# Kernel optimization log

Hardware: AMD Instinct MI355X
Metric: run time of the kernel (lower is better)

Reference implementation:

```python
import jax, jax.numpy as jnp
import numpy as np

N = 100000
FEAT = 32
RS, RT = 128, 100
BOUND = 1.6
K_A = -2.0 * np.log(0.2)  # thresholds from module-level constants
K_B = -2.0 * np.log(0.8)


def setup_inputs() -> dict:
    key = jax.random.key(0)
    ks = jax.random.split(key, 10)
    pts = jax.random.normal(ks[0], (N, 3), dtype=jnp.float32) * 0.5
    time = jax.random.uniform(ks[1], (N, 1), dtype=jnp.float32)
    # build well-conditioned SPD covariances, then extract the 6 unique entries
    A = jax.random.normal(ks[2], (N, 3, 3), dtype=jnp.float32) * 0.3
    C = A @ jnp.swapaxes(A, 1, 2) + 0.05 * jnp.eye(3, dtype=jnp.float32)
    cov6 = jnp.stack([C[:, 0, 0], C[:, 0, 1], C[:, 0, 2],
                      C[:, 1, 1], C[:, 1, 2], C[:, 2, 2]], axis=-1)
    planes = {}
    shapes = {0: (FEAT, RS, RS), 1: (FEAT, RS, RS), 2: (FEAT, RS, RT),
              3: (FEAT, RS, RS), 4: (FEAT, RS, RT), 5: (FEAT, RS, RT)}
    for i in range(6):
        planes[f'plane{i}'] = jax.random.normal(ks[3 + i], shapes[i], dtype=jnp.float32) * 0.1
    return dict(pts=pts, time=time, cov6=cov6, **planes)


def _cov3x3(c6):
    # [N,6] -> symmetric [N,3,3]
    r0 = jnp.stack([c6[:, 0], c6[:, 1], c6[:, 2]], axis=-1)
    r1 = jnp.stack([c6[:, 1], c6[:, 3], c6[:, 4]], axis=-1)
    r2 = jnp.stack([c6[:, 2], c6[:, 4], c6[:, 5]], axis=-1)
    return jnp.stack([r0, r1, r2], axis=1)


def _structured_samples(pts, cov6):
    # faithful to structured_gaussian_samples (offsets computed under no_grad)
    sg = jax.lax.stop_gradient
    C = _cov3x3(sg(cov6))
    _, V = jnp.linalg.eigh(C)                      # eigenvectors as columns
    normals = V.reshape(-1, 3)                     # rows of V, as in .view(-1,1,3)
    Cinv = jnp.linalg.inv(C)
    Cinv_rep = jnp.repeat(Cinv, 3, axis=0)         # [3N,3,3]
    lam = jnp.einsum('ni,nij,nj->n', normals, Cinv_rep, normals)[:, None]
    p_a = jnp.sqrt(K_A / lam) * normals
    p_b = jnp.sqrt(K_B / lam) * normals
    o = jnp.repeat(sg(pts), 3, axis=0)             # [3N,3]
    x_a = sg((o + p_a).reshape(-1, 3, 3))
    x_b = sg((o + p_b).reshape(-1, 3, 3))
    x_an = sg((o - p_a).reshape(-1, 3, 3))
    x_bn = sg((o - p_b).reshape(-1, 3, 3))
    return jnp.concatenate([pts[:, None, :], x_a, x_b, x_an, x_bn], axis=1)  # [N,13,3]


def _bilinear(plane, coords):
    # plane [F,H,W]; coords [M,2] in [-1,1], coord0 -> W (x), coord1 -> H (y); align_corners=True
    F_, H, W = plane.shape
    x = (coords[:, 0] + 1.0) * 0.5 * (W - 1)
    y = (coords[:, 1] + 1.0) * 0.5 * (H - 1)
    x0 = jnp.floor(x); y0 = jnp.floor(y)
    wx = (x - x0)[:, None]; wy = (y - y0)[:, None]
    x0i = jnp.clip(x0, 0, W - 1).astype(jnp.int32)
    x1i = jnp.clip(x0 + 1, 0, W - 1).astype(jnp.int32)
    y0i = jnp.clip(y0, 0, H - 1).astype(jnp.int32)
    y1i = jnp.clip(y0 + 1, 0, H - 1).astype(jnp.int32)
    v00 = plane[:, y0i, x0i].T  # [M,F]
    v01 = plane[:, y0i, x1i].T
    v10 = plane[:, y1i, x0i].T
    v11 = plane[:, y1i, x1i].T
    return ((1 - wy) * ((1 - wx) * v00 + wx * v01)
            + wy * ((1 - wx) * v10 + wx * v11))


def _forward(pts, time, cov6, planes):
    M = 13
    samples = _structured_samples(pts, cov6)          # [N,13,3]
    t = time * 2.0 - 1.0
    t = jnp.tile(t, (samples.shape[1], 1))            # faithful to time.repeat(13,1)
    aabb_max = jnp.full((3,), BOUND, dtype=pts.dtype)
    aabb_min = jnp.full((3,), -BOUND, dtype=pts.dtype)
    s = (samples - aabb_max) * (2.0 / (aabb_min - aabb_max)) - 1.0  # normalize_aabb
    data = jnp.concatenate([s.reshape(-1, 3), t], axis=-1)  # [13N,4]
    coord_pairs = [(0, 1), (0, 2), (3, 0), (1, 2), (3, 1), (3, 2)]
    space = 1.0
    spacetime = 1.0
    for i, (q, r) in enumerate(coord_pairs):
        feat = _bilinear(planes[i], data[:, (q, r)])  # [13N,F]
        feat = feat.reshape(-1, M, feat.shape[-1]).mean(axis=1)  # [N,F]
        if i in (0, 1, 3):
            space = space * feat
        else:
            spacetime = spacetime * feat
    return space, spacetime


def reference(pts, time, cov6, plane0, plane1, plane2, plane3, plane4, plane5):
    space, spacetime = _forward(pts, time, cov6,
                                [plane0, plane1, plane2, plane3, plane4, plane5])
    coltime = jnp.ones((), dtype=space.dtype)
    return space, spacetime, coltime
```

## Files before the change

### kernel.cpp

```cpp
#include <hip/hip_runtime.h>
#include <hip/hip_fp16.h>
#include <stdint.h>

#define NP 100000
#define PPB 64
#define KA 3.2188758248682006f
#define KB 0.44628710262841953f
#define PSCALE 16.0f

#define SS_DW 131072
#define ST_DW 102400
#define OFF0 0
#define OFF1 (OFF0 + SS_DW)
#define OFF2 (OFF1 + SS_DW)
#define OFF3 (OFF2 + ST_DW)
#define OFF4 (OFF3 + SS_DW)
#define OFF5 (OFF4 + ST_DW)

typedef float v2f __attribute__((ext_vector_type(2)));
typedef __fp16 v2h __attribute__((ext_vector_type(2)));

__device__ __forceinline__ int clampi(int v, int hi){ v = v < 0 ? 0 : v; return v > hi ? hi : v; }

struct Dim { int i0, i1; float fr; };

__device__ __forceinline__ Dim mkdim(float g, int hi){
  float fl = floorf(g);
  Dim d;
  d.fr = g - fl;
  int i = (int)fl;
  d.i0 = clampi(i, hi);
  d.i1 = clampi(i + 1, hi);
  return d;
}

template<bool HI>
__device__ __forceinline__ __half2 dec8(uint32_t w){
#if __has_builtin(__builtin_amdgcn_cvt_scalef32_pk_f16_fp8)
  v2h h = __builtin_amdgcn_cvt_scalef32_pk_f16_fp8(w, 1.0f, HI);
  return __builtin_bit_cast(__half2, h);
#else
  v2f f = __builtin_amdgcn_cvt_pk_f32_fp8((int)w, HI);
  v2h h = __builtin_amdgcn_cvt_pkrtz(f.x, f.y);
  return __builtin_bit_cast(__half2, h);
#endif
}

__device__ __forceinline__ void row8(uint4 v, __half2 w, __half2* acc){
  acc[0] = __hfma2(dec8<false>(v.x), w, acc[0]);
  acc[1] = __hfma2(dec8<true >(v.x), w, acc[1]);
  acc[2] = __hfma2(dec8<false>(v.y), w, acc[2]);
  acc[3] = __hfma2(dec8<true >(v.y), w, acc[3]);
  acc[4] = __hfma2(dec8<false>(v.z), w, acc[4]);
  acc[5] = __hfma2(dec8<true >(v.z), w, acc[5]);
  acc[6] = __hfma2(dec8<false>(v.w), w, acc[6]);
  acc[7] = __hfma2(dec8<true >(v.w), w, acc[7]);
}

__device__ __forceinline__ void bilinpair(const uint4* __restrict__ P,
    int rA, int rB, int x0, __half2 wx, __half2 wyg, __half2 wyf,
    int fp, __half2* acc){
  uint4 vA = P[((rA + x0) << 1) + fp];
  uint4 vB = P[((rB + x0) << 1) + fp];
  __half2 wA = __hmul2(wyg, wx), wB = __hmul2(wyf, wx);
  row8(vA, wA, acc);
  row8(vB, wB, acc);
}

__device__ __forceinline__ float3 eigvec3(float c00,float c01,float c02,
                                          float c11,float c12,float c22,float lam){
  float m00 = c00 - lam, m11 = c11 - lam, m22 = c22 - lam;
  float ux0 = c01*c12 - c02*m11, uy0 = c02*c01 - m00*c12, uz0 = m00*m11 - c01*c01;
  float ux1 = c01*m22 - c02*c12, uy1 = c02*c02 - m00*m22, uz1 = m00*c12 - c01*c02;
  float ux2 = m11*m22 - c12*c12, uy2 = c12*c02 - c01*m22, uz2 = c01*c12 - m11*c02;
  float n0 = ux0*ux0 + uy0*uy0 + uz0*uz0;
  float n1 = ux1*ux1 + uy1*uy1 + uz1*uz1;
  float n2 = ux2*ux2 + uy2*uy2 + uz2*uz2;
  float ux = ux0, uy = uy0, uz = uz0, nn = n0;
  if (n1 > nn){ ux = ux1; uy = uy1; uz = uz1; nn = n1; }
  if (n2 > nn){ ux = ux2; uy = uy2; uz = uz2; nn = n2; }
  float inv = 1.0f / sqrtf(nn + 1e-45f);
  return make_float3(ux*inv, uy*inv, uz*inv);
}

__global__ __launch_bounds__(256) void wpf_transpose(
    const float* __restrict__ p0, const float* __restrict__ p1,
    const float* __restrict__ p2, const float* __restrict__ p3,
    const float* __restrict__ p4, const float* __restrict__ p5,
    uint32_t* __restrict__ ws, float* __restrict__ coltime)
{
  __shared__ float tile[32][65];
  int plane = blockIdx.y;
  if (plane == 0 && blockIdx.x == 0 && threadIdx.x == 0) coltime[0] = 1.0f;
  const float* src; int off, HW;
  switch (plane){
    case 0:  src = p0; off = OFF0; HW = 16384; break;
    case 1:  src = p1; off = OFF1; HW = 16384; break;
    case 2:  src = p2; off = OFF2; HW = 12800; break;
    case 3:  src = p3; off = OFF3; HW = 16384; break;
    case 4:  src = p4; off = OFF4; HW = 12800; break;
    default: src = p5; off = OFF5; HW = 12800; break;
  }
  int hw0 = blockIdx.x * 64;
  if (hw0 >= HW) return;
  int hwt = threadIdx.x & 63;
  int fq  = threadIdx.x >> 6;
  #pragma unroll
  for (int i = 0; i < 8; ++i){
    int f = fq * 8 + i;
    tile[f][hwt] = src[f * HW + hw0 + hwt];
  }
  __syncthreads();
  int d  = threadIdx.x & 7;
  int h2 = threadIdx.x >> 3;
  #pragma unroll
  for (int i = 0; i < 2; ++i){
    int hl = i * 32 + h2;
    float a = tile[4*d+0][hl] * PSCALE;
    float b = tile[4*d+1][hl] * PSCALE;
    float c = tile[4*d+2][hl] * PSCALE;
    float e = tile[4*d+3][hl] * PSCALE;
    int r = __builtin_amdgcn_cvt_pk_fp8_f32(a, b, 0, false);
    r     = __builtin_amdgcn_cvt_pk_fp8_f32(c, e, r, true);
    ws[off + (hw0 + hl) * 8 + d] = (uint32_t)r;
  }
}

__global__ __launch_bounds__(256, 4) void wpf_main(
    const float* __restrict__ pts, const float* __restrict__ tim,
    const float* __restrict__ cov6, const uint32_t* __restrict__ ws,
    float* __restrict__ out)
{
  __shared__ float4 smp[PPB][13];
  int tidl = threadIdx.x;
  int pbase = blockIdx.x * PPB;

  if (tidl < PPB){
    int pt = pbase + tidl;
    if (pt < NP){
      float px = pts[pt*3+0], py = pts[pt*3+1], pz = pts[pt*3+2];
      float c00 = cov6[pt*6+0], c01 = cov6[pt*6+1], c02 = cov6[pt*6+2];
      float c11 = cov6[pt*6+3], c12 = cov6[pt*6+4], c22 = cov6[pt*6+5];

      float q3 = (c00 + c11 + c22) * (1.0f/3.0f);
      float p1 = c01*c01 + c02*c02 + c12*c12;
      float d00 = c00 - q3, d11 = c11 - q3, d22 = c22 - q3;
      float p2 = d00*d00 + d11*d11 + d22*d22 + 2.0f*p1;
      float pp = sqrtf(p2 * (1.0f/6.0f)) + 1e-30f;
      float pinv = 1.0f / pp;
      float b00 = d00*pinv, b11 = d11*pinv, b22 = d22*pinv;
      float b01 = c01*pinv, b02 = c02*pinv, b12 = c12*pinv;
      float detB = b00*(b11*b22 - b12*b12) - b01*(b01*b22 - b12*b02) + b02*(b01*b12 - b11*b02);
      float r = fminf(1.0f, fmaxf(-1.0f, 0.5f * detB));
      float phi = acosf(r) * (1.0f/3.0f);
      float l2 = q3 + 2.0f*pp*cosf(phi);
      float l0 = q3 + 2.0f*pp*cosf(phi + 2.0943951023931953f);
      float3 v0 = eigvec3(c00,c01,c02,c11,c12,c22, l0);
      float3 v2 = eigvec3(c00,c01,c02,c11,c12,c22, l2);
      float v1x = v2.y*v0.z - v2.z*v0.y;
      float v1y = v2.z*v0.x - v2.x*v0.z;
      float v1z = v2.x*v0.y - v2.y*v0.x;
      float v1inv = 1.0f / sqrtf(v1x*v1x + v1y*v1y + v1z*v1z + 1e-45f);
      v1x *= v1inv; v1y *= v1inv; v1z *= v1inv;

      float nx[3] = { v0.x, v0.y, v0.z };
      float ny[3] = { v1x,  v1y,  v1z  };
      float nz[3] = { v2.x, v2.y, v2.z };

      float A00 = c11*c22 - c12*c12;
      float A01 = c02*c12 - c01*c22;
      float A02 = c01*c12 - c02*c11;
      float A11 = c00*c22 - c02*c02;
      float A12 = c01*c02 - c00*c12;
      float A22 = c00*c11 - c01*c01;
      float det  = c00*A00 + c01*A01 + c02*A02;
      float dinv = 1.0f / det;
      float i00 = A00*dinv, i01 = A01*dinv, i02 = A02*dinv;
      float i11 = A11*dinv, i12 = A12*dinv, i22 = A22*dinv;

      float gpx = fmaf(px, -39.6875f, 63.5f);
      float gpy = fmaf(py, -39.6875f, 63.5f);
      float gpz = fmaf(pz, -39.6875f, 63.5f);
      float axA[3], ayA[3], azA[3], axB[3], ayB[3], azB[3];
      #pragma unroll
      for (int k = 0; k < 3; ++k){
        float a = nx[k], b = ny[k], c = nz[k];
        float lam = i00*a*a + i11*b*b + i22*c*c + 2.0f*(i01*a*b + i02*a*c + i12*b*c);
        float linv = 1.0f / lam;
        float sA = -39.6875f * sqrtf(KA * linv);
        float sB = -39.6875f * sqrtf(KB * linv);
        axA[k] = sA*a; ayA[k] = sA*b; azA[k] = sA*c;
        axB[k] = sB*a; ayB[k] = sB*b; azB[k] = sB*c;
      }

      int tb = (pt * 13) % NP;
      int ti = tb;
      smp[tidl][0] = make_float4(gpx, gpy, gpz, tim[ti] * 99.0f);
      #pragma unroll
      for (int k = 0; k < 3; ++k){
        ti = tb + 1 + k; if (ti >= NP) ti -= NP;
        smp[tidl][1+k]  = make_float4(gpx+axA[k], gpy+ayA[k], gpz+azA[k], tim[ti]*99.0f);
      }
      #pragma unroll
      for (int k = 0; k < 3; ++k){
        ti = tb + 4 + k; if (ti >= NP) ti -= NP;
        smp[tidl][4+k]  = make_float4(gpx+axB[k], gpy+ayB[k], gpz+azB[k], tim[ti]*99.0f);
      }
      #pragma unroll
      for (int k = 0; k < 3; ++k){
        ti = tb + 7 + k; if (ti >= NP) ti -= NP;
        smp[tidl][7+k]  = make_float4(gpx-axA[k], gpy-ayA[k], gpz-azA[k], tim[ti]*99.0f);
      }
      #pragma unroll
      for (int k = 0; k < 3; ++k){
        ti = tb + 10 + k; if (ti >= NP) ti -= NP;
        smp[tidl][10+k] = make_float4(gpx-axB[k], gpy-ayB[k], gpz-azB[k], tim[ti]*99.0f);
      }
    }
  }
  __syncthreads();

  int lp = tidl >> 2, fp = tidl & 3;
  int pt = pbase + lp;
  if (pt >= NP) return;
  bool xhi = (fp & 2) != 0;

  const uint4* __restrict__ w0p = reinterpret_cast<const uint4*>(ws + OFF0);
  const uint4* __restrict__ w1p = reinterpret_cast<const uint4*>(ws + OFF1);
  const uint4* __restrict__ w2p = reinterpret_cast<const uint4*>(ws + OFF2);
  const uint4* __restrict__ w3p = reinterpret_cast<const uint4*>(ws + OFF3);
  const uint4* __restrict__ w4p = reinterpret_cast<const uint4*>(ws + OFF4);
  const uint4* __restrict__ w5p = reinterpret_cast<const uint4*>(ws + OFF5);

  __half2 acc[6][8];
  __half2 z = __float2half2_rn(0.0f);
  #pragma unroll
  for (int i = 0; i < 6; ++i)
    #pragma unroll
    for (int j = 0; j < 8; ++j) acc[i][j] = z;

  #pragma unroll 2
  for (int m = 0; m < 13; ++m){
    float4 s = smp[lp][m];
    Dim d0 = mkdim(s.x, 127);
    Dim d1 = mkdim(s.y, 127);
    Dim d2 = mkdim(s.z, 127);
    Dim dt = mkdim(s.w, 99);

    float f0x = (d0.i0 == d0.i1) ? 0.0f : d0.fr;
    float f1x = (d1.i0 == d1.i1) ? 0.0f : d1.fr;
    float ftx = (dt.i0 == dt.i1) ? 0.0f : dt.fr;

    __half2 f0h = __float2half2_rn(d0.fr), g0h = __float2half2_rn(1.0f - d0.fr);
    __half2 f1h = __float2half2_rn(d1.fr), g1h = __float2half2_rn(1.0f - d1.fr);
    __half2 f2h = __float2half2_rn(d2.fr), g2h = __float2half2_rn(1.0f - d2.fr);

    __half2 wx0 = __float2half2_rn(xhi ? f0x : 1.0f - f0x);
    __half2 wx1 = __float2half2_rn(xhi ? f1x : 1.0f - f1x);
    __half2 wxt = __float2half2_rn(xhi ? ftx : 1.0f - ftx);

    int r1a = d1.i0 << 7, r1b = d1.i1 << 7;
    int r2a = d2.i0 << 7, r2b = d2.i1 << 7;
    int q0a = d0.i0 * 100, q0b = d0.i1 * 100;
    int q1a = d1.i0 * 100, q1b = d1.i1 * 100;
    int q2a = d2.i0 * 100, q2b = d2.i1 * 100;

    bilinpair(w0p, r1a, r1b, d0.i0, wx0, g1h, f1h, fp, acc[0]);
    bilinpair(w1p, r2a, r2b, d0.i0, wx0, g2h, f2h, fp, acc[1]);
    bilinpair(w2p, q0a, q0b, dt.i0, wxt, g0h, f0h, fp, acc[2]);
    bilinpair(w3p, r2a, r2b, d1.i0, wx1, g2h, f2h, fp, acc[3]);
    bilinpair(w4p, q1a, q1b, dt.i0, wxt, g1h, f1h, fp, acc[4]);
    bilinpair(w5p, q2a, q2b, dt.i0, wxt, g2h, f2h, fp, acc[5]);
  }

  #pragma unroll
  for (int i = 0; i < 6; ++i)
    #pragma unroll
    for (int j = 0; j < 8; ++j){
      int o = __shfl_xor(__builtin_bit_cast(int, acc[i][j]), 2);
      acc[i][j] = __hadd2(acc[i][j], __builtin_bit_cast(__half2, o));
    }

  if (fp < 2){
    const float s13 = 1.0f / (13.0f * PSCALE);
    float sp[16], st[16];
    #pragma unroll
    for (int j = 0; j < 8; ++j){
      float2 a0 = __half22float2(acc[0][j]);
      float2 a1 = __half22float2(acc[1][j]);
      float2 a2 = __half22float2(acc[2][j]);
      float2 a3 = __half22float2(acc[3][j]);
      float2 a4 = __half22float2(acc[4][j]);
      float2 a5 = __half22float2(acc[5][j]);
      sp[2*j]   = (a0.x*s13)*(a1.x*s13)*(a3.x*s13);
      sp[2*j+1] = (a0.y*s13)*(a1.y*s13)*(a3.y*s13);
      st[2*j]   = (a2.x*s13)*(a4.x*s13)*(a5.x*s13);
      st[2*j+1] = (a2.y*s13)*(a4.y*s13)*(a5.y*s13);
    }
    float* osp = out + pt*32 + fp*16;
    float* ost = osp + NP*32;
    #pragma unroll
    for (int q = 0; q < 4; ++q){
      reinterpret_cast<float4*>(osp)[q] = make_float4(sp[4*q], sp[4*q+1], sp[4*q+2], sp[4*q+3]);
      reinterpret_cast<float4*>(ost)[q] = make_float4(st[4*q], st[4*q+1], st[4*q+2], st[4*q+3]);
    }
  }
}

extern "C" void kernel_launch(void* const* d_in, const int* in_sizes, int n_in,
                              void* d_out, int out_size, void* d_ws, size_t ws_size,
                              hipStream_t stream) {
  (void)in_sizes; (void)n_in; (void)out_size; (void)ws_size;
  const float* pts  = (const float*)d_in[0];
  const float* tim  = (const float*)d_in[1];
  const float* cov6 = (const float*)d_in[2];
  const float* p0 = (const float*)d_in[3];
  const float* p1 = (const float*)d_in[4];
  const float* p2 = (const float*)d_in[5];
  const float* p3 = (const float*)d_in[6];
  const float* p4 = (const float*)d_in[7];
  const float* p5 = (const float*)d_in[8];
  float* out = (float*)d_out;
  uint32_t* ws = (uint32_t*)d_ws;

  dim3 tgrid(256, 6);
  wpf_transpose<<<tgrid, 256, 0, stream>>>(p0, p1, p2, p3, p4, p5, ws, out + 2*NP*32);

  int nblk = (NP + PPB - 1) / PPB;
  wpf_main<<<nblk, 256, 0, stream>>>(pts, tim, cov6, ws, out);
}
```

Baseline: 174.6 us.

## Split per-point geometry into separate kernel writing sample records to workspace

Moves the eigen-decomposition and sample generation out of the main kernel into a dedicated kernel that uses all 256 threads per block (previously only 64 of 256 threads did this work while the rest waited at a barrier). The results go to a global workspace buffer in a sample-major layout, and the gather kernel reads them directly instead of from shared memory. The gather kernel drops the shared-memory array and raises its occupancy hint to 8. The cost is an extra kernel launch plus a round trip of about 20 MB through global memory/L2, and each sample record is loaded redundantly by four threads.

```diff
diff --git a/kernel.cpp b/kernel.cpp
--- a/kernel.cpp
+++ b/kernel.cpp
@@ -3,7 +3,6 @@
 #include <stdint.h>
 
 #define NP 100000
-#define PPB 64
 #define KA 3.2188758248682006f
 #define KB 0.44628710262841953f
 #define PSCALE 16.0f
@@ -16,6 +15,7 @@
 #define OFF3 (OFF2 + ST_DW)
 #define OFF4 (OFF3 + SS_DW)
 #define OFF5 (OFF4 + ST_DW)
+#define REC_OFF (OFF5 + ST_DW)
 
 typedef float v2f __attribute__((ext_vector_type(2)));
 typedef __fp16 v2h __attribute__((ext_vector_type(2)));
@@ -126,102 +126,99 @@
   }
 }
 
-__global__ __launch_bounds__(256, 4) void wpf_main(
+__global__ __launch_bounds__(256) void wpf_geom(
     const float* __restrict__ pts, const float* __restrict__ tim,
-    const float* __restrict__ cov6, const uint32_t* __restrict__ ws,
+    const float* __restrict__ cov6, float4* __restrict__ rec)
+{
+  int pt = blockIdx.x * 256 + threadIdx.x;
+  if (pt >= NP) return;
+
+  float px = pts[pt*3+0], py = pts[pt*3+1], pz = pts[pt*3+2];
+  float c00 = cov6[pt*6+0], c01 = cov6[pt*6+1], c02 = cov6[pt*6+2];
+  float c11 = cov6[pt*6+3], c12 = cov6[pt*6+4], c22 = cov6[pt*6+5];
+
+  float q3 = (c00 + c11 + c22) * (1.0f/3.0f);
+  float p1 = c01*c01 + c02*c02 + c12*c12;
+  float d00 = c00 - q3, d11 = c11 - q3, d22 = c22 - q3;
+  float p2 = d00*d00 + d11*d11 + d22*d22 + 2.0f*p1;
+  float pp = sqrtf(p2 * (1.0f/6.0f)) + 1e-30f;
+  float pinv = 1.0f / pp;
+  float b00 = d00*pinv, b11 = d11*pinv, b22 = d22*pinv;
+  float b01 = c01*pinv, b02 = c02*pinv, b12 = c12*pinv;
+  float detB = b00*(b11*b22 - b12*b12) - b01*(b01*b22 - b12*b02) + b02*(b01*b12 - b11*b02);
+  float r = fminf(1.0f, fmaxf(-1.0f, 0.5f * detB));
+  float phi = acosf(r) * (1.0f/3.0f);
+  float l2 = q3 + 2.0f*pp*cosf(phi);
+  float l0 = q3 + 2.0f*pp*cosf(phi + 2.0943951023931953f);
+  float3 v0 = eigvec3(c00,c01,c02,c11,c12,c22, l0);
+  float3 v2 = eigvec3(c00,c01,c02,c11,c12,c22, l2);
+  float v1x = v2.y*v0.z - v2.z*v0.y;
+  float v1y = v2.z*v0.x - v2.x*v0.z;
+  float v1z = v2.x*v0.y - v2.y*v0.x;
+  float v1inv = 1.0f / sqrtf(v1x*v1x + v1y*v1y + v1z*v1z + 1e-45f);
+  v1x *= v1inv; v1y *= v1inv; v1z *= v1inv;
+
+  float nx[3] = { v0.x, v0.y, v0.z };
+  float ny[3] = { v1x,  v1y,  v1z  };
+  float nz[3] = { v2.x, v2.y, v2.z };
+
+  float A00 = c11*c22 - c12*c12;
+  float A01 = c02*c12 - c01*c22;
+  float A02 = c01*c12 - c02*c11;
+  float A11 = c00*c22 - c02*c02;
+  float A12 = c01*c02 - c00*c12;
+  float A22 = c00*c11 - c01*c01;
+  float det  = c00*A00 + c01*A01 + c02*A02;
+  float dinv = 1.0f / det;
+  float i00 = A00*dinv, i01 = A01*dinv, i02 = A02*dinv;
+  float i11 = A11*dinv, i12 = A12*dinv, i22 = A22*dinv;
+
+  float gpx = fmaf(px, -39.6875f, 63.5f);
+  float gpy = fmaf(py, -39.6875f, 63.5f);
+  float gpz = fmaf(pz, -39.6875f, 63.5f);
+  float axA[3], ayA[3], azA[3], axB[3], ayB[3], azB[3];
+  #pragma unroll
+  for (int k = 0; k < 3; ++k){
+    float a = nx[k], b = ny[k], c = nz[k];
+    float lam = i00*a*a + i11*b*b + i22*c*c + 2.0f*(i01*a*b + i02*a*c + i12*b*c);
+    float linv = 1.0f / lam;
+    float sA = -39.6875f * sqrtf(KA * linv);
+    float sB = -39.6875f * sqrtf(KB * linv);
+    axA[k] = sA*a; ayA[k] = sA*b; azA[k] = sA*c;
+    axB[k] = sB*a; ayB[k] = sB*b; azB[k] = sB*c;
+  }
+
+  int tb = (pt * 13) % NP;
+  int ti = tb;
+  rec[0*NP + pt] = make_float4(gpx, gpy, gpz, tim[ti] * 99.0f);
+  #pragma unroll
+  for (int k = 0; k < 3; ++k){
+    ti = tb + 1 + k; if (ti >= NP) ti -= NP;
+    rec[(1+k)*NP + pt]  = make_float4(gpx+axA[k], gpy+ayA[k], gpz+azA[k], tim[ti]*99.0f);
+  }
+  #pragma unroll
+  for (int k = 0; k < 3; ++k){
+    ti = tb + 4 + k; if (ti >= NP) ti -= NP;
+    rec[(4+k)*NP + pt]  = make_float4(gpx+axB[k], gpy+ayB[k], gpz+azB[k], tim[ti]*99.0f);
+  }
+  #pragma unroll
+  for (int k = 0; k < 3; ++k){
+    ti = tb + 7 + k; if (ti >= NP) ti -= NP;
+    rec[(7+k)*NP + pt]  = make_float4(gpx-axA[k], gpy-ayA[k], gpz-azA[k], tim[ti]*99.0f);
+  }
+  #pragma unroll
+  for (int k = 0; k < 3; ++k){
+    ti = tb + 10 + k; if (ti >= NP) ti -= NP;
+    rec[(10+k)*NP + pt] = make_float4(gpx-axB[k], gpy-ayB[k], gpz-azB[k], tim[ti]*99.0f);
+  }
+}
+
+__global__ __launch_bounds__(256, 8) void wpf_gather(
+    const float4* __restrict__ rec, const uint32_t* __restrict__ ws,
     float* __restrict__ out)
 {
-  __shared__ float4 smp[PPB][13];
-  int tidl = threadIdx.x;
-  int pbase = blockIdx.x * PPB;
-
-  if (tidl < PPB){
-    int pt = pbase + tidl;
-    if (pt < NP){
-      float px = pts[pt*3+0], py = pts[pt*3+1], pz = pts[pt*3+2];
-      float c00 = cov6[pt*6+0], c01 = cov6[pt*6+1], c02 = cov6[pt*6+2];
-      float c11 = cov6[pt*6+3], c12 = cov6[pt*6+4], c22 = cov6[pt*6+5];
-
-      float q3 = (c00 + c11 + c22) * (1.0f/3.0f);
-      float p1 = c01*c01 + c02*c02 + c12*c12;
-      float d00 = c00 - q3, d11 = c11 - q3, d22 = c22 - q3;
-      float p2 = d00*d00 + d11*d11 + d22*d22 + 2.0f*p1;
-      float pp = sqrtf(p2 * (1.0f/6.0f)) + 1e-30f;
-      float pinv = 1.0f / pp;
-      float b00 = d00*pinv, b11 = d11*pinv, b22 = d22*pinv;
-      float b01 = c01*pinv, b02 = c02*pinv, b12 = c12*pinv;
-      float detB = b00*(b11*b22 - b12*b12) - b01*(b01*b22 - b12*b02) + b02*(b01*b12 - b11*b02);
-      float r = fminf(1.0f, fmaxf(-1.0f, 0.5f * detB));
-      float phi = acosf(r) * (1.0f/3.0f);
-      float l2 = q3 + 2.0f*pp*cosf(phi);
-      float l0 = q3 + 2.0f*pp*cosf(phi + 2.0943951023931953f);
-      float3 v0 = eigvec3(c00,c01,c02,c11,c12,c22, l0);
-      float3 v2 = eigvec3(c00,c01,c02,c11,c12,c22, l2);
-      float v1x = v2.y*v0.z - v2.z*v0.y;
-      float v1y = v2.z*v0.x - v2.x*v0.z;
-      float v1z = v2.x*v0.y - v2.y*v0.x;
-      float v1inv = 1.0f / sqrtf(v1x*v1x + v1y*v1y + v1z*v1z + 1e-45f);
-      v1x *= v1inv; v1y *= v1inv; v1z *= v1inv;
-
-      float nx[3] = { v0.x, v0.y, v0.z };
-      float ny[3] = { v1x,  v1y,  v1z  };
-      float nz[3] = { v2.x, v2.y, v2.z };
-
-      float A00 = c11*c22 - c12*c12;
-      float A01 = c02*c12 - c01*c22;
-      float A02 = c01*c12 - c02*c11;
-      float A11 = c00*c22 - c02*c02;
-      float A12 = c01*c02 - c00*c12;
-      float A22 = c00*c11 - c01*c01;
-      float det  = c00*A00 + c01*A01 + c02*A02;
-      float dinv = 1.0f / det;
-      float i00 = A00*dinv, i01 = A01*dinv, i02 = A02*dinv;
-      float i11 = A11*dinv, i12 = A12*dinv, i22 = A22*dinv;
-
-      float gpx = fmaf(px, -39.6875f, 63.5f);
-      float gpy = fmaf(py, -39.6875f, 63.5f);
-      float gpz = fmaf(pz, -39.6875f, 63.5f);
-      float axA[3], ayA[3], azA[3], axB[3], ayB[3], azB[3];
-      #pragma unroll
-      for (int k = 0; k < 3; ++k){
-        float a = nx[k], b = ny[k], c = nz[k];
-        float lam = i00*a*a + i11*b*b + i22*c*c + 2.0f*(i01*a*b + i02*a*c + i12*b*c);
-        float linv = 1.0f / lam;
-        float sA = -39.6875f * sqrtf(KA * linv);
-        float sB = -39.6875f * sqrtf(KB * linv);
-        axA[k] = sA*a; ayA[k] = sA*b; azA[k] = sA*c;
-        axB[k] = sB*a; ayB[k] = sB*b; azB[k] = sB*c;
-      }
-
-      int tb = (pt * 13) % NP;
-      int ti = tb;
-      smp[tidl][0] = make_float4(gpx, gpy, gpz, tim[ti] * 99.0f);
-      #pragma unroll
-      for (int k = 0; k < 3; ++k){
-        ti = tb + 1 + k; if (ti >= NP) ti -= NP;
-        smp[tidl][1+k]  = make_float4(gpx+axA[k], gpy+ayA[k], gpz+azA[k], tim[ti]*99.0f);
-      }
-      #pragma unroll
-      for (int k = 0; k < 3; ++k){
-        ti = tb + 4 + k; if (ti >= NP) ti -= NP;
-        smp[tidl][4+k]  = make_float4(gpx+axB[k], gpy+ayB[k], gpz+azB[k], tim[ti]*99.0f);
-      }
-      #pragma unroll
-      for (int k = 0; k < 3; ++k){
-        ti = tb + 7 + k; if (ti >= NP) ti -= NP;
-        smp[tidl][7+k]  = make_float4(gpx-axA[k], gpy-ayA[k], gpz-azA[k], tim[ti]*99.0f);
-      }
-      #pragma unroll
-      for (int k = 0; k < 3; ++k){
-        ti = tb + 10 + k; if (ti >= NP) ti -= NP;
-        smp[tidl][10+k] = make_float4(gpx-axB[k], gpy-ayB[k], gpz-azB[k], tim[ti]*99.0f);
-      }
-    }
-  }
-  __syncthreads();
-
-  int lp = tidl >> 2, fp = tidl & 3;
-  int pt = pbase + lp;
+  int tid = blockIdx.x * 256 + threadIdx.x;
+  int pt = tid >> 2, fp = tid & 3;
   if (pt >= NP) return;
   bool xhi = (fp & 2) != 0;
 
@@ -241,7 +238,7 @@
 
   #pragma unroll 2
   for (int m = 0; m < 13; ++m){
-    float4 s = smp[lp][m];
+    float4 s = rec[m*NP + pt];
     Dim d0 = mkdim(s.x, 127);
     Dim d1 = mkdim(s.y, 127);
     Dim d2 = mkdim(s.z, 127);
@@ -322,10 +319,13 @@
   const float* p5 = (const float*)d_in[8];
   float* out = (float*)d_out;
   uint32_t* ws = (uint32_t*)d_ws;
+  float4* rec = reinterpret_cast<float4*>(ws + REC_OFF);
 
   dim3 tgrid(256, 6);
   wpf_transpose<<<tgrid, 256, 0, stream>>>(p0, p1, p2, p3, p4, p5, ws, out + 2*NP*32);
 
-  int nblk = (NP + PPB - 1) / PPB;
-  wpf_main<<<nblk, 256, 0, stream>>>(pts, tim, cov6, ws, out);
-}
+  wpf_geom<<<(NP + 255) / 256, 256, 0, stream>>>(pts, tim, cov6, rec);
+
+  int nthreads = NP * 4;
+  wpf_gather<<<(nthreads + 255) / 256, 256, 0, stream>>>(rec, ws, out);
+}
```

New measurement: 368.7 us. 2.11x slower.

## Split bilinear y-corners across lanes: 8 threads per point, 32 points per block

Applied to the files above, without the earlier changes.

Each point now gets 8 lanes instead of 4. The extra lane bit selects the y-corner row, so each lane issues one 16-byte gather per plane per sample instead of two. A second xor-shuffle reduction over lane bit 4 then combines the two y-corners. The block now covers 32 points, which doubles the grid and halves per-lane load and FMA work, in exchange for twice the sample-setup duplication, an extra shuffle pass, and only 32 of 256 threads doing the eigen setup. Bounds checks are dropped because NP divides evenly by 32.

```diff
diff --git a/kernel.cpp b/kernel.cpp
--- a/kernel.cpp
+++ b/kernel.cpp
@@ -3,7 +3,7 @@
 #include <stdint.h>
 
 #define NP 100000
-#define PPB 64
+#define PPB 32
 #define KA 3.2188758248682006f
 #define KB 0.44628710262841953f
 #define PSCALE 16.0f
@@ -55,16 +55,6 @@
   acc[5] = __hfma2(dec8<true >(v.z), w, acc[5]);
   acc[6] = __hfma2(dec8<false>(v.w), w, acc[6]);
   acc[7] = __hfma2(dec8<true >(v.w), w, acc[7]);
-}
-
-__device__ __forceinline__ void bilinpair(const uint4* __restrict__ P,
-    int rA, int rB, int x0, __half2 wx, __half2 wyg, __half2 wyf,
-    int fp, __half2* acc){
-  uint4 vA = P[((rA + x0) << 1) + fp];
-  uint4 vB = P[((rB + x0) << 1) + fp];
-  __half2 wA = __hmul2(wyg, wx), wB = __hmul2(wyf, wx);
-  row8(vA, wA, acc);
-  row8(vB, wB, acc);
 }
 
 __device__ __forceinline__ float3 eigvec3(float c00,float c01,float c02,
@@ -137,93 +127,92 @@
 
   if (tidl < PPB){
     int pt = pbase + tidl;
-    if (pt < NP){
-      float px = pts[pt*3+0], py = pts[pt*3+1], pz = pts[pt*3+2];
-      float c00 = cov6[pt*6+0], c01 = cov6[pt*6+1], c02 = cov6[pt*6+2];
-      float c11 = cov6[pt*6+3], c12 = cov6[pt*6+4], c22 = cov6[pt*6+5];
-
-      float q3 = (c00 + c11 + c22) * (1.0f/3.0f);
-      float p1 = c01*c01 + c02*c02 + c12*c12;
-      float d00 = c00 - q3, d11 = c11 - q3, d22 = c22 - q3;
-      float p2 = d00*d00 + d11*d11 + d22*d22 + 2.0f*p1;
-      float pp = sqrtf(p2 * (1.0f/6.0f)) + 1e-30f;
-      float pinv = 1.0f / pp;
-      float b00 = d00*pinv, b11 = d11*pinv, b22 = d22*pinv;
-      float b01 = c01*pinv, b02 = c02*pinv, b12 = c12*pinv;
-      float detB = b00*(b11*b22 - b12*b12) - b01*(b01*b22 - b12*b02) + b02*(b01*b12 - b11*b02);
-      float r = fminf(1.0f, fmaxf(-1.0f, 0.5f * detB));
-      float phi = acosf(r) * (1.0f/3.0f);
-      float l2 = q3 + 2.0f*pp*cosf(phi);
-      float l0 = q3 + 2.0f*pp*cosf(phi + 2.0943951023931953f);
-      float3 v0 = eigvec3(c00,c01,c02,c11,c12,c22, l0);
-      float3 v2 = eigvec3(c00,c01,c02,c11,c12,c22, l2);
-      float v1x = v2.y*v0.z - v2.z*v0.y;
-      float v1y = v2.z*v0.x - v2.x*v0.z;
-      float v1z = v2.x*v0.y - v2.y*v0.x;
-      float v1inv = 1.0f / sqrtf(v1x*v1x + v1y*v1y + v1z*v1z + 1e-45f);
-      v1x *= v1inv; v1y *= v1inv; v1z *= v1inv;
-
-      float nx[3] = { v0.x, v0.y, v0.z };
-      float ny[3] = { v1x,  v1y,  v1z  };
-      float nz[3] = { v2.x, v2.y, v2.z };
-
-      float A00 = c11*c22 - c12*c12;
-      float A01 = c02*c12 - c01*c22;
-      float A02 = c01*c12 - c02*c11;
-      float A11 = c00*c22 - c02*c02;
-      float A12 = c01*c02 - c00*c12;
-      float A22 = c00*c11 - c01*c01;
-      float det  = c00*A00 + c01*A01 + c02*A02;
-      float dinv = 1.0f / det;
-      float i00 = A00*dinv, i01 = A01*dinv, i02 = A02*dinv;
-      float i11 = A11*dinv, i12 = A12*dinv, i22 = A22*dinv;
-
-      float gpx = fmaf(px, -39.6875f, 63.5f);
-      float gpy = fmaf(py, -39.6875f, 63.5f);
-      float gpz = fmaf(pz, -39.6875f, 63.5f);
-      float axA[3], ayA[3], azA[3], axB[3], ayB[3], azB[3];
-      #pragma unroll
-      for (int k = 0; k < 3; ++k){
-        float a = nx[k], b = ny[k], c = nz[k];
-        float lam = i00*a*a + i11*b*b + i22*c*c + 2.0f*(i01*a*b + i02*a*c + i12*b*c);
-        float linv = 1.0f / lam;
-        float sA = -39.6875f * sqrtf(KA * linv);
-        float sB = -39.6875f * sqrtf(KB * linv);
-        axA[k] = sA*a; ayA[k] = sA*b; azA[k] = sA*c;
-        axB[k] = sB*a; ayB[k] = sB*b; azB[k] = sB*c;
-      }
-
-      int tb = (pt * 13) % NP;
-      int ti = tb;
-      smp[tidl][0] = make_float4(gpx, gpy, gpz, tim[ti] * 99.0f);
-      #pragma unroll
-      for (int k = 0; k < 3; ++k){
-        ti = tb + 1 + k; if (ti >= NP) ti -= NP;
-        smp[tidl][1+k]  = make_float4(gpx+axA[k], gpy+ayA[k], gpz+azA[k], tim[ti]*99.0f);
-      }
-      #pragma unroll
-      for (int k = 0; k < 3; ++k){
-        ti = tb + 4 + k; if (ti >= NP) ti -= NP;
-        smp[tidl][4+k]  = make_float4(gpx+axB[k], gpy+ayB[k], gpz+azB[k], tim[ti]*99.0f);
-      }
-      #pragma unroll
-      for (int k = 0; k < 3; ++k){
-        ti = tb + 7 + k; if (ti >= NP) ti -= NP;
-        smp[tidl][7+k]  = make_float4(gpx-axA[k], gpy-ayA[k], gpz-azA[k], tim[ti]*99.0f);
-      }
-      #pragma unroll
-      for (int k = 0; k < 3; ++k){
-        ti = tb + 10 + k; if (ti >= NP) ti -= NP;
-        smp[tidl][10+k] = make_float4(gpx-axB[k], gpy-ayB[k], gpz-azB[k], tim[ti]*99.0f);
-      }
+    float px = pts[pt*3+0], py = pts[pt*3+1], pz = pts[pt*3+2];
+    float c00 = cov6[pt*6+0], c01 = cov6[pt*6+1], c02 = cov6[pt*6+2];
+    float c11 = cov6[pt*6+3], c12 = cov6[pt*6+4], c22 = cov6[pt*6+5];
+
+    float q3 = (c00 + c11 + c22) * (1.0f/3.0f);
+    float p1 = c01*c01 + c02*c02 + c12*c12;
+    float d00 = c00 - q3, d11 = c11 - q3, d22 = c22 - q3;
+    float p2 = d00*d00 + d11*d11 + d22*d22 + 2.0f*p1;
+    float pp = sqrtf(p2 * (1.0f/6.0f)) + 1e-30f;
+    float pinv = 1.0f / pp;
+    float b00 = d00*pinv, b11 = d11*pinv, b22 = d22*pinv;
+    float b01 = c01*pinv, b02 = c02*pinv, b12 = c12*pinv;
+    float detB = b00*(b11*b22 - b12*b12) - b01*(b01*b22 - b12*b02) + b02*(b01*b12 - b11*b02);
+    float r = fminf(1.0f, fmaxf(-1.0f, 0.5f * detB));
+    float phi = acosf(r) * (1.0f/3.0f);
+    float l2 = q3 + 2.0f*pp*cosf(phi);
+    float l0 = q3 + 2.0f*pp*cosf(phi + 2.0943951023931953f);
+    float3 v0 = eigvec3(c00,c01,c02,c11,c12,c22, l0);
+    float3 v2 = eigvec3(c00,c01,c02,c11,c12,c22, l2);
+    float v1x = v2.y*v0.z - v2.z*v0.y;
+    float v1y = v2.z*v0.x - v2.x*v0.z;
+    float v1z = v2.x*v0.y - v2.y*v0.x;
+    float v1inv = 1.0f / sqrtf(v1x*v1x + v1y*v1y + v1z*v1z + 1e-45f);
+    v1x *= v1inv; v1y *= v1inv; v1z *= v1inv;
+
+    float nx[3] = { v0.x, v0.y, v0.z };
+    float ny[3] = { v1x,  v1y,  v1z  };
+    float nz[3] = { v2.x, v2.y, v2.z };
+
+    float A00 = c11*c22 - c12*c12;
+    float A01 = c02*c12 - c01*c22;
+    float A02 = c01*c12 - c02*c11;
+    float A11 = c00*c22 - c02*c02;
+    float A12 = c01*c02 - c00*c12;
+    float A22 = c00*c11 - c01*c01;
+    float det  = c00*A00 + c01*A01 + c02*A02;
+    float dinv = 1.0f / det;
+    float i00 = A00*dinv, i01 = A01*dinv, i02 = A02*dinv;
+    float i11 = A11*dinv, i12 = A12*dinv, i22 = A22*dinv;
+
+    float gpx = fmaf(px, -39.6875f, 63.5f);
+    float gpy = fmaf(py, -39.6875f, 63.5f);
+    float gpz = fmaf(pz, -39.6875f, 63.5f);
+    float axA[3], ayA[3], azA[3], axB[3], ayB[3], azB[3];
+    #pragma unroll
+    for (int k = 0; k < 3; ++k){
+      float a = nx[k], b = ny[k], c = nz[k];
+      float lam = i00*a*a + i11*b*b + i22*c*c + 2.0f*(i01*a*b + i02*a*c + i12*b*c);
+      float linv = 1.0f / lam;
+      float sA = -39.6875f * sqrtf(KA * linv);
+      float sB = -39.6875f * sqrtf(KB * linv);
+      axA[k] = sA*a; ayA[k] = sA*b; azA[k] = sA*c;
+      axB[k] = sB*a; ayB[k] = sB*b; azB[k] = sB*c;
+    }
+
+    int tb = (pt * 13) % NP;
+    int ti = tb;
+    smp[tidl][0] = make_float4(gpx, gpy, gpz, tim[ti] * 99.0f);
+    #pragma unroll
+    for (int k = 0; k < 3; ++k){
+      ti = tb + 1 + k; if (ti >= NP) ti -= NP;
+      smp[tidl][1+k]  = make_float4(gpx+axA[k], gpy+ayA[k], gpz+azA[k], tim[ti]*99.0f);
+    }
+    #pragma unroll
+    for (int k = 0; k < 3; ++k){
+      ti = tb + 4 + k; if (ti >= NP) ti -= NP;
+      smp[tidl][4+k]  = make_float4(gpx+axB[k], gpy+ayB[k], gpz+azB[k], tim[ti]*99.0f);
+    }
+    #pragma unroll
+    for (int k = 0; k < 3; ++k){
+      ti = tb + 7 + k; if (ti >= NP) ti -= NP;
+      smp[tidl][7+k]  = make_float4(gpx-axA[k], gpy-ayA[k], gpz-azA[k], tim[ti]*99.0f);
+    }
+    #pragma unroll
+    for (int k = 0; k < 3; ++k){
+      ti = tb + 10 + k; if (ti >= NP) ti -= NP;
+      smp[tidl][10+k] = make_float4(gpx-axB[k], gpy-ayB[k], gpz-azB[k], tim[ti]*99.0f);
     }
   }
   __syncthreads();
 
-  int lp = tidl >> 2, fp = tidl & 3;
+  int lp = tidl >> 3, fp = tidl & 7;
   int pt = pbase + lp;
-  if (pt >= NP) return;
   bool xhi = (fp & 2) != 0;
+  bool yhi = (fp & 4) != 0;
+  int q = fp & 3;
 
   const uint4* __restrict__ w0p = reinterpret_cast<const uint4*>(ws + OFF0);
   const uint4* __restrict__ w1p = reinterpret_cast<const uint4*>(ws + OFF1);
@@ -251,26 +240,29 @@
     float f1x = (d1.i0 == d1.i1) ? 0.0f : d1.fr;
     float ftx = (dt.i0 == dt.i1) ? 0.0f : dt.fr;
 
-    __half2 f0h = __float2half2_rn(d0.fr), g0h = __float2half2_rn(1.0f - d0.fr);
-    __half2 f1h = __float2half2_rn(d1.fr), g1h = __float2half2_rn(1.0f - d1.fr);
-    __half2 f2h = __float2half2_rn(d2.fr), g2h = __float2half2_rn(1.0f - d2.fr);
-
-    __half2 wx0 = __float2half2_rn(xhi ? f0x : 1.0f - f0x);
-    __half2 wx1 = __float2half2_rn(xhi ? f1x : 1.0f - f1x);
-    __half2 wxt = __float2half2_rn(xhi ? ftx : 1.0f - ftx);
-
-    int r1a = d1.i0 << 7, r1b = d1.i1 << 7;
-    int r2a = d2.i0 << 7, r2b = d2.i1 << 7;
-    int q0a = d0.i0 * 100, q0b = d0.i1 * 100;
-    int q1a = d1.i0 * 100, q1b = d1.i1 * 100;
-    int q2a = d2.i0 * 100, q2b = d2.i1 * 100;
-
-    bilinpair(w0p, r1a, r1b, d0.i0, wx0, g1h, f1h, fp, acc[0]);
-    bilinpair(w1p, r2a, r2b, d0.i0, wx0, g2h, f2h, fp, acc[1]);
-    bilinpair(w2p, q0a, q0b, dt.i0, wxt, g0h, f0h, fp, acc[2]);
-    bilinpair(w3p, r2a, r2b, d1.i0, wx1, g2h, f2h, fp, acc[3]);
-    bilinpair(w4p, q1a, q1b, dt.i0, wxt, g1h, f1h, fp, acc[4]);
-    bilinpair(w5p, q2a, q2b, dt.i0, wxt, g2h, f2h, fp, acc[5]);
+    float wx0 = xhi ? f0x : 1.0f - f0x;
+    float wx1 = xhi ? f1x : 1.0f - f1x;
+    float wxt = xhi ? ftx : 1.0f - ftx;
+    float wy0 = yhi ? d0.fr : 1.0f - d0.fr;
+    float wy1 = yhi ? d1.fr : 1.0f - d1.fr;
+    float wy2 = yhi ? d2.fr : 1.0f - d2.fr;
+    int yi0 = yhi ? d0.i1 : d0.i0;
+    int yi1 = yhi ? d1.i1 : d1.i0;
+    int yi2 = yhi ? d2.i1 : d2.i0;
+
+    __half2 w0 = __float2half2_rn(wx0 * wy1);
+    __half2 w1 = __float2half2_rn(wx0 * wy2);
+    __half2 w2 = __float2half2_rn(wxt * wy0);
+    __half2 w3 = __float2half2_rn(wx1 * wy2);
+    __half2 w4 = __float2half2_rn(wxt * wy1);
+    __half2 w5 = __float2half2_rn(wxt * wy2);
+
+    row8(w0p[(((yi1 << 7) + d0.i0) << 1) + q], w0, acc[0]);
+    row8(w1p[(((yi2 << 7) + d0.i0) << 1) + q], w1, acc[1]);
+    row8(w2p[(((yi0 * 100) + dt.i0) << 1) + q], w2, acc[2]);
+    row8(w3p[(((yi2 << 7) + d1.i0) << 1) + q], w3, acc[3]);
+    row8(w4p[(((yi1 * 100) + dt.i0) << 1) + q], w4, acc[4]);
+    row8(w5p[(((yi2 * 100) + dt.i0) << 1) + q], w5, acc[5]);
   }
 
   #pragma unroll
@@ -278,6 +270,13 @@
     #pragma unroll
     for (int j = 0; j < 8; ++j){
       int o = __shfl_xor(__builtin_bit_cast(int, acc[i][j]), 2);
+      acc[i][j] = __hadd2(acc[i][j], __builtin_bit_cast(__half2, o));
+    }
+  #pragma unroll
+  for (int i = 0; i < 6; ++i)
+    #pragma unroll
+    for (int j = 0; j < 8; ++j){
+      int o = __shfl_xor(__builtin_bit_cast(int, acc[i][j]), 4);
       acc[i][j] = __hadd2(acc[i][j], __builtin_bit_cast(__half2, o));
     }
 
@@ -300,9 +299,9 @@
     float* osp = out + pt*32 + fp*16;
     float* ost = osp + NP*32;
     #pragma unroll
-    for (int q = 0; q < 4; ++q){
-      reinterpret_cast<float4*>(osp)[q] = make_float4(sp[4*q], sp[4*q+1], sp[4*q+2], sp[4*q+3]);
-      reinterpret_cast<float4*>(ost)[q] = make_float4(st[4*q], st[4*q+1], st[4*q+2], st[4*q+3]);
+    for (int qq = 0; qq < 4; ++qq){
+      reinterpret_cast<float4*>(osp)[qq] = make_float4(sp[4*qq], sp[4*qq+1], sp[4*qq+2], sp[4*qq+3]);
+      reinterpret_cast<float4*>(ost)[qq] = make_float4(st[4*qq], st[4*qq+1], st[4*qq+2], st[4*qq+3]);
     }
   }
 }
@@ -326,6 +325,5 @@
   dim3 tgrid(256, 6);
   wpf_transpose<<<tgrid, 256, 0, stream>>>(p0, p1, p2, p3, p4, p5, ws, out + 2*NP*32);
 
-  int nblk = (NP + PPB - 1) / PPB;
-  wpf_main<<<nblk, 256, 0, stream>>>(pts, tim, cov6, ws, out);
-}
+  wpf_main<<<NP / PPB, 256, 0, stream>>>(pts, tim, cov6, ws, out);
+}
```

Result: no change. 172.7 us (-1.1%).
